# Performance work log

Measured on AMD Instinct MI355X. Metric: run time of the kernel, lower is better.

Reference implementation:

```python
import jax, jax.numpy as jnp
import numpy as np

DIM = 2240; HEADS = 20; HD = 112
B = 1; F = 8; H = 16; W = 28; S = F * H * W; ENC = 300
HID = int(3.0 * DIM)  # 6720
EPS_LN = 1e-6; EPS_RMS = 1e-5


def setup_inputs():
    ks = iter(jax.random.split(jax.random.key(0), 64))
    nrm = lambda shape, s=1.0: jax.random.normal(next(ks), shape, jnp.float32) * s
    wsc = 0.02
    inp = dict(
        hidden_states=nrm((B, S, DIM)),
        encoder_hidden_states=nrm((B, ENC, DIM)),
        timestep=nrm((B, 6 * DIM), 0.1),
        freqs_cos=nrm((1, S, 1, HD)),
        freqs_sin=nrm((1, S, 1, HD)),
        scale_shift_table=nrm((6, DIM), 1.0 / np.sqrt(DIM)),
    )
    for p in ("a1", "a2"):
        inp[p + "_qw"] = nrm((DIM, DIM), wsc); inp[p + "_qb"] = jnp.zeros((DIM,), jnp.float32)
        inp[p + "_kw"] = nrm((DIM, DIM), wsc); inp[p + "_kb"] = jnp.zeros((DIM,), jnp.float32)
        inp[p + "_vw"] = nrm((DIM, DIM), wsc); inp[p + "_vb"] = jnp.zeros((DIM,), jnp.float32)
        inp[p + "_nq"] = jnp.ones((DIM,), jnp.float32)
        inp[p + "_nk"] = jnp.ones((DIM,), jnp.float32)
        inp[p + "_ow"] = nrm((DIM, DIM), wsc); inp[p + "_ob"] = jnp.zeros((DIM,), jnp.float32)
    inp["ff_inv_w"] = nrm((1, 1, DIM, 2 * HID), wsc)
    inp["ff_inv_b"] = jnp.zeros((2 * HID,), jnp.float32)
    inp["ff_depth_w"] = nrm((3, 3, 1, 2 * HID), wsc)
    inp["ff_depth_b"] = jnp.zeros((2 * HID,), jnp.float32)
    inp["ff_point_w"] = nrm((1, 1, HID, DIM), wsc)
    inp["ff_temp_w"] = nrm((3, 1, DIM, DIM), wsc)
    inp["frames"] = F; inp["height"] = H; inp["width"] = W
    return inp


def _ln(x):  # LayerNorm, no affine (elementwise_affine=False)
    m = jnp.mean(x, -1, keepdims=True)
    v = jnp.mean((x - m) ** 2, -1, keepdims=True)
    return (x - m) * jax.lax.rsqrt(v + EPS_LN)


def _rms(x, w):  # rms_norm_across_heads on full inner dim
    return x * jax.lax.rsqrt(jnp.mean(x * x, -1, keepdims=True) + EPS_RMS) * w


def _rope(x, cos, sin):  # interleaved rotary as in SanaLinearAttnProcessor3_0
    x1, x2 = x[..., 0::2], x[..., 1::2]
    c, s = cos[..., 0::2], sin[..., 1::2]
    out = jnp.stack([x1 * c - x2 * s, x1 * s + x2 * c], axis=-1)
    return out.reshape(x.shape)


def _conv(x, k, padding, groups=1):
    return jax.lax.conv_general_dilated(
        x, k, (1, 1), padding,
        dimension_numbers=("NHWC", "HWIO", "NHWC"),
        feature_group_count=groups)


def _linear_attn(x, qw, qb, kw, kb, vw, vb, nq, nk, ow, ob, cos, sin):
    b, s, _ = x.shape
    q = jax.nn.relu(_rms(x @ qw + qb, nq)).reshape(b, s, HEADS, HD)
    k = jax.nn.relu(_rms(x @ kw + kb, nk)).reshape(b, s, HEADS, HD)
    v = (x @ vw + vb).reshape(b, s, HEADS, HD)
    qr, kr = _rope(q, cos, sin), _rope(k, cos, sin)
    ksum = jnp.sum(k, axis=1)                             # [b,h,d] (un-rotated)
    denom = jnp.einsum("bhd,bshd->bsh", ksum, q) + 1e-15  # z^{-1}
    scores = jnp.einsum("bshe,bshd->bhed", v, kr)         # [b,h,dv,d]
    out = jnp.einsum("bhed,bshd->bshe", scores, qr) / denom[..., None]
    return out.reshape(b, s, HEADS * HD) @ ow + ob


def _cross_attn(x, enc, qw, qb, kw, kb, vw, vb, nq, nk, ow, ob):
    b, s, _ = x.shape; t = enc.shape[1]
    q = _rms(x @ qw + qb, nq).reshape(b, s, HEADS, HD)
    k = _rms(enc @ kw + kb, nk).reshape(b, t, HEADS, HD)
    v = (enc @ vw + vb).reshape(b, t, HEADS, HD)
    logits = jnp.einsum("bshd,bthd->bhst", q, k) / np.sqrt(HD).astype(np.float32)
    attn = jax.nn.softmax(logits, axis=-1)
    out = jnp.einsum("bhst,bthd->bshd", attn, v).reshape(b, s, HEADS * HD)
    return out @ ow + ob


def _ff(x, inv_w, inv_b, depth_w, depth_b, point_w, temp_w, f, h, w):
    b = x.shape[0]
    y = x.reshape(b * f, h, w, DIM)
    y = jax.nn.silu(_conv(y, inv_w, "SAME") + inv_b)
    y = _conv(y, depth_w, "SAME", groups=2 * HID) + depth_b
    a, g = y[..., :HID], y[..., HID:]
    y = _conv(a * jax.nn.silu(g), point_w, "SAME")        # [bf,h,w,DIM]
    yt = y.reshape(b, f, h * w, DIM)                      # conv over frames axis
    yt = yt + _conv(yt, temp_w, ((1, 1), (0, 0)))
    return yt.reshape(b, f, h, w, DIM)


def reference(hidden_states, encoder_hidden_states, timestep, freqs_cos, freqs_sin,
              scale_shift_table,
              a1_qw, a1_qb, a1_kw, a1_kb, a1_vw, a1_vb, a1_nq, a1_nk, a1_ow, a1_ob,
              a2_qw, a2_qb, a2_kw, a2_kb, a2_vw, a2_vb, a2_nq, a2_nk, a2_ow, a2_ob,
              ff_inv_w, ff_inv_b, ff_depth_w, ff_depth_b, ff_point_w, ff_temp_w,
              frames, height, width):
    b = hidden_states.shape[0]
    mods = scale_shift_table[None] + timestep.reshape(b, 6, DIM)
    sh_msa, sc_msa, g_msa, sh_mlp, sc_mlp, g_mlp = jnp.split(mods, 6, axis=1)
    nh = _ln(hidden_states) * (1 + sc_msa) + sh_msa
    attn = _linear_attn(nh, a1_qw, a1_qb, a1_kw, a1_kb, a1_vw, a1_vb,
                        a1_nq, a1_nk, a1_ow, a1_ob, freqs_cos, freqs_sin)
    x = hidden_states + g_msa * attn
    x = x + _cross_attn(x, encoder_hidden_states, a2_qw, a2_qb, a2_kw, a2_kb,
                        a2_vw, a2_vb, a2_nq, a2_nk, a2_ow, a2_ob)
    nh = _ln(x) * (1 + sc_mlp) + sh_mlp
    ff = _ff(nh.reshape(b, frames, height, width, DIM),
             ff_inv_w, ff_inv_b, ff_depth_w, ff_depth_b, ff_point_w, ff_temp_w,
             frames, height, width)
    x = x + g_mlp * ff.reshape(b, frames * height * width, DIM)
    return x
```

## Files before the change

kernel.cpp:

```cpp
#include <hip/hip_runtime.h>

#define DIMC 2240
#define STOK 3584
#define ENCT 300
#define NH   20
#define HDIM 112
#define HID1 6720
#define HID2 13440
#define DD   (2240*2240)
#define SD   (3584*2240)

typedef short bf16x8 __attribute__((ext_vector_type(8)));
typedef float f32x4  __attribute__((ext_vector_type(4)));

__device__ __forceinline__ unsigned short f2bf(float f){
  unsigned int u = __float_as_uint(f);
  u += 0x7fffu + ((u >> 16) & 1u);
  return (unsigned short)(u >> 16);
}
__device__ __forceinline__ float bf2f(unsigned short h){
  return __uint_as_float(((unsigned int)h) << 16);
}
__device__ __forceinline__ void gl_lds16(const unsigned short* g, unsigned short* l){
  __builtin_amdgcn_global_load_lds(
      (const __attribute__((address_space(1))) unsigned int*)(const void*)g,
      (__attribute__((address_space(3))) unsigned int*)(void*)l, 16, 0, 0);
}

__global__ void cvt_k(const float4* __restrict__ src, ushort4* __restrict__ dst, int n4){
  int i = blockIdx.x*256 + threadIdx.x;
  if (i < n4){
    float4 v = src[i];
    ushort4 o; o.x = f2bf(v.x); o.y = f2bf(v.y); o.z = f2bf(v.z); o.w = f2bf(v.w);
    dst[i] = o;
  }
}

__global__ __launch_bounds__(256) void cvtT3_k(const float* __restrict__ s0,
    const float* __restrict__ s1, const float* __restrict__ s2,
    unsigned short* __restrict__ dst, int rows, int ldsrc, int c0, int nc,
    int ldd, long long dzoff){
  const float* src = (blockIdx.z == 0) ? s0 : ((blockIdx.z == 1) ? s1 : s2);
  unsigned short* d = dst + (size_t)blockIdx.z * (size_t)dzoff;
  __shared__ float tile[32][33];
  const int tx = threadIdx.x & 31, ty = threadIdx.x >> 5;
  const int colBase = blockIdx.x*32;
  #pragma unroll
  for (int i = 0; i < 4; ++i){
    int rr = blockIdx.y*32 + ty + i*8;
    int cc = colBase + tx;
    tile[ty + i*8][tx] = (cc < nc) ? src[(size_t)rr*ldsrc + c0 + cc] : 0.f;
  }
  __syncthreads();
  #pragma unroll
  for (int i = 0; i < 4; ++i){
    int n = colBase + ty + i*8;
    int k = blockIdx.y*32 + tx;
    d[(size_t)n*ldd + k] = f2bf(tile[tx][ty + i*8]);
  }
}

__global__ void zpad_k(unsigned short* __restrict__ m0, unsigned short* __restrict__ m1){
  int i = blockIdx.x*256 + threadIdx.x;
  if (i < 125440){
    reinterpret_cast<uint4*>(m0)[i] = make_uint4(0u,0u,0u,0u);
    reinterpret_cast<uint4*>(m1)[i] = make_uint4(0u,0u,0u,0u);
  }
}

__global__ void pack3_k(float* __restrict__ dst, const float* __restrict__ b0,
    const float* __restrict__ b1, const float* __restrict__ b2, int nslots){
  int i = blockIdx.x*256 + threadIdx.x;
  if (i >= nslots*2304) return;
  int slot = i / 2304, d = i - slot*2304;
  const float* src = (slot == 0) ? b0 : ((slot == 1) ? b1 : b2);
  dst[i] = (d < 2240) ? src[d] : 0.f;
}

__global__ void mods_k(const float* __restrict__ sst, const float* __restrict__ ts, float* __restrict__ mods){
  int i = blockIdx.x*256 + threadIdx.x;
  if (i < 6*DIMC) mods[i] = sst[i] + ts[i];
}

__global__ __launch_bounds__(256) void ln_mod_k(const float* __restrict__ x,
    const float* __restrict__ mods, int shj, int scj, unsigned short* __restrict__ out)
{
  const int s = blockIdx.x;
  const float4* row4 = reinterpret_cast<const float4*>(x + (size_t)s*DIMC);
  const float4* sh4 = reinterpret_cast<const float4*>(mods + shj*DIMC);
  const float4* sc4 = reinterpret_cast<const float4*>(mods + scj*DIMC);
  float sum = 0.f, sq = 0.f;
  for (int o = threadIdx.x; o < 560; o += 256){
    float4 v = row4[o];
    sum += v.x + v.y + v.z + v.w;
    sq  += v.x*v.x + v.y*v.y + v.z*v.z + v.w*v.w;
  }
  #pragma unroll
  for (int o = 32; o; o >>= 1){ sum += __shfl_down(sum, o); sq += __shfl_down(sq, o); }
  __shared__ float sA[4], sB[4];
  int w = threadIdx.x >> 6, l = threadIdx.x & 63;
  if (!l){ sA[w] = sum; sB[w] = sq; }
  __syncthreads();
  sum = sA[0]+sA[1]+sA[2]+sA[3];
  sq  = sB[0]+sB[1]+sB[2]+sB[3];
  float mean = sum * (1.f/DIMC);
  float rs = rsqrtf(sq*(1.f/DIMC) - mean*mean + 1e-6f);
  unsigned short* orow = out + (size_t)s*DIMC;
  for (int o = threadIdx.x; o < 560; o += 256){
    float4 v = row4[o], sc = sc4[o], sh = sh4[o];
    ushort4 r;
    r.x = f2bf((v.x-mean)*rs*(1.f + sc.x) + sh.x);
    r.y = f2bf((v.y-mean)*rs*(1.f + sc.y) + sh.y);
    r.z = f2bf((v.z-mean)*rs*(1.f + sc.z) + sh.z);
    r.w = f2bf((v.w-mean)*rs*(1.f + sc.w) + sh.w);
    *reinterpret_cast<ushort4*>(orow + o*4) = r;
  }
}

template<int RELU, int ROPE>
__global__ __launch_bounds__(256) void rms_bf_k(unsigned short* __restrict__ x, const float* __restrict__ nw,
    const float* __restrict__ cosb, const float* __restrict__ sinb, unsigned short* __restrict__ xr)
{
  const int s = blockIdx.x;
  unsigned short* row = x + (size_t)s*DIMC;
  float sq = 0.f;
  for (int o = threadIdx.x; o < 280; o += 256){
    uint4 v = *reinterpret_cast<const uint4*>(row + o*8);
    unsigned int uu[4] = {v.x, v.y, v.z, v.w};
    #pragma unroll
    for (int j = 0; j < 4; ++j){
      float lo = bf2f((unsigned short)(uu[j] & 0xffffu));
      float hi = bf2f((unsigned short)(uu[j] >> 16));
      sq += lo*lo + hi*hi;
    }
  }
  #pragma unroll
  for (int o = 32; o; o >>= 1) sq += __shfl_down(sq, o);
  __shared__ float sB[4];
  int w = threadIdx.x >> 6, l = threadIdx.x & 63;
  if (!l) sB[w] = sq;
  __syncthreads();
  sq = sB[0]+sB[1]+sB[2]+sB[3];
  float rs = rsqrtf(sq*(1.f/DIMC) + 1e-5f);
  for (int o = threadIdx.x; o < 280; o += 256){
    uint4 v = *reinterpret_cast<const uint4*>(row + o*8);
    unsigned int uu[4] = {v.x, v.y, v.z, v.w};
    float4 n0 = *reinterpret_cast<const float4*>(nw + o*8);
    float4 n1 = *reinterpret_cast<const float4*>(nw + o*8 + 4);
    float nn[8] = {n0.x,n0.y,n0.z,n0.w,n1.x,n1.y,n1.z,n1.w};
    float vals[8];
    #pragma unroll
    for (int j = 0; j < 4; ++j){
      vals[2*j]   = bf2f((unsigned short)(uu[j] & 0xffffu))*rs*nn[2*j];
      vals[2*j+1] = bf2f((unsigned short)(uu[j] >> 16))*rs*nn[2*j+1];
    }
    if constexpr (RELU){
      #pragma unroll
      for (int j = 0; j < 8; ++j) vals[j] = fmaxf(vals[j], 0.f);
    }
    uint4 o1;
    unsigned int* po = &o1.x;
    #pragma unroll
    for (int j = 0; j < 4; ++j)
      po[j] = (unsigned int)f2bf(vals[2*j]) | ((unsigned int)f2bf(vals[2*j+1]) << 16);
    *reinterpret_cast<uint4*>(row + o*8) = o1;
    if constexpr (ROPE){
      int jb = (o*8) % HDIM;
      uint4 o2;
      unsigned int* pr = &o2.x;
      #pragma unroll
      for (int p = 0; p < 4; ++p){
        float c  = cosb[(size_t)s*HDIM + jb + 2*p];
        float sn = sinb[(size_t)s*HDIM + jb + 2*p + 1];
        float r0 = vals[2*p]*c - vals[2*p+1]*sn;
        float r1 = vals[2*p]*sn + vals[2*p+1]*c;
        pr[p] = (unsigned int)f2bf(r0) | ((unsigned int)f2bf(r1) << 16);
      }
      *reinterpret_cast<uint4*>(xr + (size_t)s*DIMC + o*8) = o2;
    }
  }
}

template<int EPI>
__global__ __launch_bounds__(256) void gemm_bt(
  const unsigned short* __restrict__ A, const unsigned short* __restrict__ Bt,
  const float* __restrict__ bias, float* __restrict__ Cf, unsigned short* __restrict__ Cb,
  const float* __restrict__ res, const float* __restrict__ gate,
  int M, int N, int K, int ldc, int PW, int lda, int tcsh)
{
  __shared__ __align__(16) unsigned short Al[128*64];
  __shared__ __align__(16) unsigned short Bl[128*64];
  const int gx = gridDim.x, gy = gridDim.y;
  const int nwg = gx*gy;
  const int orig = blockIdx.y*gx + blockIdx.x;
  const int qq = nwg >> 3, rr = nwg & 7;
  const int xcd = orig & 7, li = orig >> 3;
  const int wg = (xcd < rr ? xcd*(qq+1) : rr*(qq+1) + (xcd-rr)*qq) + li;
  const int ppw = gy*PW;
  const int panel = wg / ppw, rm = wg - panel*ppw;
  const int mrow = rm / PW;
  const int m0 = mrow*128;
  const int n0 = (panel*PW + (rm - mrow*PW))*128;

  const int t = threadIdx.x, lane = t & 63, w = t >> 6;
  const int wr = w >> 1, wc = w & 1;
  const int l16 = lane & 15, lk = lane >> 4;

  const int lr8 = lane >> 3;
  const int sc  = (lane & 7) ^ lr8;
  const unsigned short* Aps[4];
  const unsigned short* Bps[4];
  #pragma unroll
  for (int i = 0; i < 4; ++i){
    int ar = m0 + w*32 + i*8 + lr8;
    int br = n0 + w*32 + i*8 + lr8;
    Aps[i] = A  + (size_t)min(ar, M-1)*lda + sc*8;
    Bps[i] = Bt + (size_t)br*K + sc*8;
  }
  unsigned short* Ad = Al + w*2048;
  unsigned short* Bd = Bl + w*2048;

  f32x4 acc[4][4] = {};
  for (int k0 = 0; k0 < K; k0 += 64){
    size_t aoff;
    if (tcsh){
      int sec = (k0 >= 4480) ? 2 : ((k0 >= 2240) ? 1 : 0);
      aoff = (size_t)(sec*448)*lda + (unsigned)(k0 - sec*2240);
    } else {
      aoff = (size_t)k0;
    }
    __syncthreads();
    #pragma unroll
    for (int i = 0; i < 4; ++i){
      gl_lds16(Aps[i] + aoff, Ad + i*512);
      gl_lds16(Bps[i] + k0,   Bd + i*512);
    }
    __syncthreads();
    #pragma unroll
    for (int kk = 0; kk < 2; ++kk){
      bf16x8 af[4], bfr[4];
      const int chb = (kk*4 + lk) ^ (l16 & 7);
      #pragma unroll
      for (int m = 0; m < 4; ++m)
        af[m] = *reinterpret_cast<const bf16x8*>(Al + (wr*64 + m*16 + l16)*64 + chb*8);
      #pragma unroll
      for (int n = 0; n < 4; ++n)
        bfr[n] = *reinterpret_cast<const bf16x8*>(Bl + (wc*64 + n*16 + l16)*64 + chb*8);
      #pragma unroll
      for (int m = 0; m < 4; ++m)
        #pragma unroll
        for (int n = 0; n < 4; ++n)
          acc[m][n] = __builtin_amdgcn_mfma_f32_16x16x32_bf16(af[m], bfr[n], acc[m][n], 0, 0, 0);
    }
  }

  const int rb = m0 + wr*64 + lk*4;
  const int cb = n0 + wc*64 + l16;
  #pragma unroll
  for (int m = 0; m < 4; ++m){
    #pragma unroll
    for (int r = 0; r < 4; ++r){
      int row = rb + m*16 + r;
      if (row >= M) continue;
      #pragma unroll
      for (int n = 0; n < 4; ++n){
        int col = cb + n*16;
        if (col >= N) continue;
        float v = acc[m][n][r];
        float bv = bias ? bias[col] : 0.f;
        if constexpr (EPI == 6){
          int slot = col / 2304;
          int d = col - slot*2304;
          if (d < 2240)
            Cb[(size_t)slot*ldc + (size_t)row*2240 + d] = f2bf(v + bv);
        } else {
          size_t idx = (size_t)row*ldc + col;
          if constexpr (EPI == 0){ Cf[idx] = v + bv; }
          else if constexpr (EPI == 1){ float u = v + bv; Cb[idx] = f2bf(u / (1.f + __expf(-u))); }
          else if constexpr (EPI == 2){ Cb[idx] = f2bf(v + bv); }
          else if constexpr (EPI == 3){ float u = res[idx] + gate[col]*(v + bv); Cf[idx] = u; Cb[idx] = f2bf(u); }
          else if constexpr (EPI == 4){ Cf[idx] = res[idx] + v + bv; }
          else { Cf[idx] += v; }
        }
      }
    }
  }
}

__global__ void colsum_k(const unsigned short* __restrict__ k, float* __restrict__ kpart){
  int d = blockIdx.x*256 + threadIdx.x;
  if (d >= DIMC) return;
  int ch = blockIdx.y, s0 = ch*128;
  float acc = 0.f;
  for (int s = s0; s < s0+128; ++s) acc += bf2f(k[(size_t)s*DIMC + d]);
  kpart[(size_t)ch*DIMC + d] = acc;
}
__global__ void ksumred_k(const float* __restrict__ kpart, float* __restrict__ ksum){
  int d = blockIdx.x*256 + threadIdx.x;
  if (d >= DIMC) return;
  float a = 0.f;
  for (int c = 0; c < 28; ++c) a += kpart[(size_t)c*DIMC + d];
  ksum[d] = a;
}
__global__ __launch_bounds__(256) void denom_k(const unsigned short* __restrict__ q,
    const float* __restrict__ ksum, float* __restrict__ denom)
{
  int s = blockIdx.x; int w = threadIdx.x >> 6, l = threadIdx.x & 63;
  for (int h = w; h < NH; h += 4){
    const unsigned short* qb = q + (size_t)s*DIMC + h*HDIM;
    const float* kb = ksum + h*HDIM;
    float v = bf2f(qb[l])*kb[l];
    if (l < 48) v += bf2f(qb[64+l])*kb[64+l];
    #pragma unroll
    for (int o = 32; o; o >>= 1) v += __shfl_down(v, o);
    if (!l) denom[s*NH + h] = v + 1e-15f;
  }
}

#define SLSC 136
__device__ __forceinline__ int sc_idx(int e, int s){
  return e*SLSC + (s ^ (((e >> 3) & 7) << 3));
}
__global__ __launch_bounds__(256) void scores_k(const unsigned short* __restrict__ v,
    const unsigned short* __restrict__ kr, float* __restrict__ part)
{
  const int h = blockIdx.x, ch = blockIdx.y;
  __shared__ __align__(16) unsigned short Vt[112*SLSC];
  __shared__ __align__(16) unsigned short Kt[112*SLSC];
  const int t = threadIdx.x, lane = t & 63, w = t >> 6;
  const int l16 = lane & 15, lk = lane >> 4;
  const int sbase = ch*128;

  for (int p = t; p < 1792; p += 256){
    int s = p / 14, oc = (p % 14) * 8;
    bf16x8 vv = *reinterpret_cast<const bf16x8*>(v  + (size_t)(sbase+s)*DIMC + h*HDIM + oc);
    bf16x8 kk = *reinterpret_cast<const bf16x8*>(kr + (size_t)(sbase+s)*DIMC + h*HDIM + oc);
    #pragma unroll
    for (int j = 0; j < 8; ++j){
      Vt[sc_idx(oc+j, s)] = (unsigned short)vv[j];
      Kt[sc_idx(oc+j, s)] = (unsigned short)kk[j];
    }
  }
  __syncthreads();

  f32x4 acc[2][7] = {};
  #pragma unroll
  for (int ks = 0; ks < 4; ++ks){
    const int sf = ks*32 + lk*8;
    bf16x8 bfrg[7];
    #pragma unroll
    for (int nt = 0; nt < 7; ++nt){
      int d = nt*16 + l16;
      bfrg[nt] = *reinterpret_cast<const bf16x8*>(&Kt[d*SLSC + (sf ^ (((d >> 3) & 7) << 3))]);
    }
    #pragma unroll
    for (int mi = 0; mi < 2; ++mi){
      int mt = w + mi*4;
      if (mt < 7){
        int e = mt*16 + l16;
        bf16x8 afrg = *reinterpret_cast<const bf16x8*>(&Vt[e*SLSC + (sf ^ (((e >> 3) & 7) << 3))]);
        #pragma unroll
        for (int nt = 0; nt < 7; ++nt)
          acc[mi][nt] = __builtin_amdgcn_mfma_f32_16x16x32_bf16(afrg, bfrg[nt], acc[mi][nt], 0, 0, 0);
      }
    }
  }

  float* pout = part + ((size_t)ch*NH + h)*12544;
  #pragma unroll
  for (int mi = 0; mi < 2; ++mi){
    int mt = w + mi*4;
    if (mt >= 7) continue;
    #pragma unroll
    for (int nt = 0; nt < 7; ++nt)
      #pragma unroll
      for (int r = 0; r < 4; ++r)
        pout[(size_t)(mt*16 + lk*4 + r)*HDIM + nt*16 + l16] = acc[mi][nt][r];
  }
}
__global__ void scred_k(const float* __restrict__ part, unsigned short* __restrict__ sc){
  int i = blockIdx.x*256 + threadIdx.x;
  if (i >= NH*HDIM*HDIM) return;
  float a = 0.f;
  #pragma unroll
  for (int c = 0; c < 28; ++c) a += part[(size_t)c*(NH*HDIM*HDIM) + i];
  sc[i] = f2bf(a);
}

__global__ __launch_bounds__(256) void linout_k(const unsigned short* __restrict__ qr,
    const unsigned short* __restrict__ scores, const float* __restrict__ denom,
    unsigned short* __restrict__ out)
{
  const int h = blockIdx.y;
  const int t = threadIdx.x, lane = t & 63, w = t >> 6;
  const int l16 = lane & 15, lk = lane >> 4;
  const int s0 = blockIdx.x*64 + w*16;
  const unsigned short* qrow = qr + (size_t)(s0 + l16)*DIMC + h*HDIM;
  const unsigned short* sb = scores + (size_t)h*12544;
  f32x4 acc[7] = {};
  #pragma unroll
  for (int ks = 0; ks < 4; ++ks){
    int d0 = ks*32 + lk*8;
    bf16x8 a = {};
    if (d0 < HDIM) a = *reinterpret_cast<const bf16x8*>(qrow + d0);
    #pragma unroll
    for (int nt = 0; nt < 7; ++nt){
      bf16x8 b = {};
      if (d0 < HDIM) b = *reinterpret_cast<const bf16x8*>(sb + (size_t)(nt*16 + l16)*HDIM + d0);
      acc[nt] = __builtin_amdgcn_mfma_f32_16x16x32_bf16(a, b, acc[nt], 0, 0, 0);
    }
  }
  #pragma unroll
  for (int r = 0; r < 4; ++r){
    int s = s0 + lk*4 + r;
    float dn = 1.f / denom[(size_t)s*NH + h];
    #pragma unroll
    for (int nt = 0; nt < 7; ++nt)
      out[(size_t)s*DIMC + h*HDIM + nt*16 + l16] = f2bf(acc[nt][r]*dn);
  }
}

__global__ __launch_bounds__(256) void xattn_k(
    const unsigned short* __restrict__ q,
    const unsigned short* __restrict__ k2,
    const unsigned short* __restrict__ v2,
    unsigned short* __restrict__ outb)
{
  const int h = blockIdx.y;
  const int w = threadIdx.x >> 6, lane = threadIdx.x & 63;
  const int l16 = lane & 15, lk = lane >> 4;
  const float scale = 0.09449111825230679f;

  __shared__ __align__(16) unsigned short Kl[64][136];
  __shared__ __align__(16) unsigned short Vl[112][72];
  __shared__ __align__(16) unsigned short Pl[4][16][72];

  bf16x8 qf[4];
  const unsigned short* qbase = q + (size_t)(blockIdx.x*64 + w*16 + l16)*DIMC + h*HDIM;
  #pragma unroll
  for (int c = 0; c < 4; ++c){
    int d0 = c*32 + lk*8;
    bf16x8 z = {};
    qf[c] = (d0 < HDIM) ? *reinterpret_cast<const bf16x8*>(qbase + d0) : z;
  }

  f32x4 lg[5][4] = {};
  #pragma unroll
  for (int c = 0; c < 5; ++c){
    const int kbase = c*64;
    const int nk = (c == 4) ? (ENCT - 256) : 64;
    __syncthreads();
    #pragma unroll
    for (int it = 0; it < 4; ++it){
      int li = it*256 + threadIdx.x;
      int key = li >> 4, d0 = (li & 15) << 3;
      uint4 val = make_uint4(0u,0u,0u,0u);
      if (key < nk && d0 < HDIM)
        val = *reinterpret_cast<const uint4*>(k2 + (size_t)(kbase+key)*DIMC + h*HDIM + d0);
      *reinterpret_cast<uint4*>(&Kl[key][d0]) = val;
    }
    __syncthreads();
    #pragma unroll
    for (int nt = 0; nt < 4; ++nt){
      #pragma unroll
      for (int ks = 0; ks < 4; ++ks){
        bf16x8 kf = *reinterpret_cast<const bf16x8*>(&Kl[nt*16 + l16][ks*32 + lk*8]);
        lg[c][nt] = __builtin_amdgcn_mfma_f32_16x16x32_bf16(qf[ks], kf, lg[c][nt], 0, 0, 0);
      }
    }
  }

  float mx[4] = {-3e38f, -3e38f, -3e38f, -3e38f};
  #pragma unroll
  for (int c = 0; c < 5; ++c)
    #pragma unroll
    for (int nt = 0; nt < 4; ++nt){
      bool valid = (c*64 + nt*16 + l16) < ENCT;
      #pragma unroll
      for (int r = 0; r < 4; ++r){
        float v = valid ? lg[c][nt][r]*scale : -3e38f;
        lg[c][nt][r] = v;
        mx[r] = fmaxf(mx[r], v);
      }
    }
  #pragma unroll
  for (int o = 1; o < 16; o <<= 1)
    #pragma unroll
    for (int r = 0; r < 4; ++r) mx[r] = fmaxf(mx[r], __shfl_xor(mx[r], o));
  float sm[4] = {0.f, 0.f, 0.f, 0.f};
  #pragma unroll
  for (int c = 0; c < 5; ++c)
    #pragma unroll
    for (int nt = 0; nt < 4; ++nt)
      #pragma unroll
      for (int r = 0; r < 4; ++r){
        float e = __expf(lg[c][nt][r] - mx[r]);
        lg[c][nt][r] = e;
        sm[r] += e;
      }
  #pragma unroll
  for (int o = 1; o < 16; o <<= 1)
    #pragma unroll
    for (int r = 0; r < 4; ++r) sm[r] += __shfl_xor(sm[r], o);
  float inv[4];
  #pragma unroll
  for (int r = 0; r < 4; ++r) inv[r] = 1.f / sm[r];

  f32x4 oacc[7] = {};
  #pragma unroll
  for (int c = 0; c < 5; ++c){
    const int kbase = c*64;
    const int nk = (c == 4) ? (ENCT - 256) : 64;
    __syncthreads();
    #pragma unroll
    for (int it = 0; it < 4; ++it){
      int li = it*256 + threadIdx.x;
      if (li < 896){
        int key = li/14, d0 = (li%14)*8;
        if (key < nk){
          bf16x8 vv = *reinterpret_cast<const bf16x8*>(v2 + (size_t)(kbase+key)*DIMC + h*HDIM + d0);
          #pragma unroll
          for (int j = 0; j < 8; ++j) Vl[d0+j][key] = (unsigned short)vv[j];
        } else {
          #pragma unroll
          for (int j = 0; j < 8; ++j) Vl[d0+j][key] = 0;
        }
      }
    }
    #pragma unroll
    for (int nt = 0; nt < 4; ++nt)
      #pragma unroll
      for (int r = 0; r < 4; ++r)
        Pl[w][lk*4 + r][nt*16 + l16] = f2bf(lg[c][nt][r]);
    __syncthreads();
    #pragma unroll
    for (int ks = 0; ks < 2; ++ks){
      bf16x8 pf = *reinterpret_cast<const bf16x8*>(&Pl[w][l16][ks*32 + lk*8]);
      #pragma unroll
      for (int n = 0; n < 7; ++n){
        bf16x8 vf = *reinterpret_cast<const bf16x8*>(&Vl[n*16 + l16][ks*32 + lk*8]);
        oacc[n] = __builtin_amdgcn_mfma_f32_16x16x32_bf16(pf, vf, oacc[n], 0, 0, 0);
      }
    }
  }

  const int orow = blockIdx.x*64 + w*16 + lk*4;
  #pragma unroll
  for (int n = 0; n < 7; ++n)
    #pragma unroll
    for (int r = 0; r < 4; ++r)
      outb[(size_t)(orow + r)*DIMC + h*HDIM + n*16 + l16] = f2bf(oacc[n][r]*inv[r]);
}

__global__ __launch_bounds__(256) void dw_k(const unsigned short* __restrict__ y1,
    const float* __restrict__ dw, const float* __restrict__ db, unsigned short* __restrict__ y2)
{
  int c = (blockIdx.y*256 + threadIdx.x)*2;
  if (c >= HID1) return;
  int bx = blockIdx.x;
  int xp = bx % 14;
  int yt = (bx / 14) & 3;
  int f  = bx / 56;
  int x0 = xp*2, y0 = yt*4;

  float wa[9][2], wg[9][2];
  #pragma unroll
  for (int tp = 0; tp < 9; ++tp){
    float2 va = *reinterpret_cast<const float2*>(dw + tp*HID2 + c);
    float2 vg = *reinterpret_cast<const float2*>(dw + tp*HID2 + c + HID1);
    wa[tp][0] = va.x; wa[tp][1] = va.y;
    wg[tp][0] = vg.x; wg[tp][1] = vg.y;
  }
  float2 ba = *reinterpret_cast<const float2*>(db + c);
  float2 bg = *reinterpret_cast<const float2*>(db + c + HID1);
  float a[4][2][2], g[4][2][2];
  #pragma unroll
  for (int r = 0; r < 4; ++r)
    #pragma unroll
    for (int cc = 0; cc < 2; ++cc){
      a[r][cc][0] = ba.x; a[r][cc][1] = ba.y;
      g[r][cc][0] = bg.x; g[r][cc][1] = bg.y;
    }

  #pragma unroll
  for (int dy6 = 0; dy6 < 6; ++dy6){
    int y = y0 - 1 + dy6;
    if ((unsigned)y >= 16u) continue;
    #pragma unroll
    for (int dxc = 0; dxc < 4; ++dxc){
      int x = x0 - 1 + dxc;
      if ((unsigned)x >= 28u) continue;
      size_t base = ((size_t)(f*16 + y)*28 + x)*HID2;
      unsigned int a01 = *reinterpret_cast<const unsigned int*>(y1 + base + c);
      unsigned int g01 = *reinterpret_cast<const unsigned int*>(y1 + base + c + HID1);
      float fa0 = bf2f((unsigned short)(a01 & 0xffffu));
      float fa1 = bf2f((unsigned short)(a01 >> 16));
      float fg0 = bf2f((unsigned short)(g01 & 0xffffu));
      float fg1 = bf2f((unsigned short)(g01 >> 16));
      #pragma unroll
      for (int r = 0; r < 4; ++r){
        int kdy = dy6 - r;
        if (kdy < 0 || kdy > 2) continue;
        #pragma unroll
        for (int cc = 0; cc < 2; ++cc){
          int kdx = dxc - cc;
          if (kdx < 0 || kdx > 2) continue;
          int tp = kdy*3 + kdx;
          a[r][cc][0] += fa0*wa[tp][0]; a[r][cc][1] += fa1*wa[tp][1];
          g[r][cc][0] += fg0*wg[tp][0]; g[r][cc][1] += fg1*wg[tp][1];
        }
      }
    }
  }
  #pragma unroll
  for (int r = 0; r < 4; ++r)
    #pragma unroll
    for (int cc = 0; cc < 2; ++cc){
      float s0 = g[r][cc][0] / (1.f + __expf(-g[r][cc][0]));
      float s1 = g[r][cc][1] / (1.f + __expf(-g[r][cc][1]));
      int pos = (f*16 + y0 + r)*28 + x0 + cc;
      unsigned int o = (unsigned int)f2bf(a[r][cc][0]*s0) | ((unsigned int)f2bf(a[r][cc][1]*s1) << 16);
      *reinterpret_cast<unsigned int*>(y2 + (size_t)pos*HID1 + c) = o;
    }
}

__global__ void final_k(const float* __restrict__ x2, const unsigned short* __restrict__ y3,
    const float* __restrict__ tc, const float* __restrict__ mods, float* __restrict__ out)
{
  int i4 = (blockIdx.x*256 + threadIdx.x)*4;
  if (i4 >= SD) return;
  int d = i4 % DIMC;
  float4 xv = *reinterpret_cast<const float4*>(x2 + i4);
  float4 tv = *reinterpret_cast<const float4*>(tc + i4);
  float4 gv = *reinterpret_cast<const float4*>(mods + 5*DIMC + d);
  ushort4 yv = *reinterpret_cast<const ushort4*>(y3 + i4);
  float4 o;
  o.x = xv.x + gv.x*(bf2f(yv.x) + tv.x);
  o.y = xv.y + gv.y*(bf2f(yv.y) + tv.y);
  o.z = xv.z + gv.z*(bf2f(yv.z) + tv.z);
  o.w = xv.w + gv.w*(bf2f(yv.w) + tv.w);
  *reinterpret_cast<float4*>(out + i4) = o;
}

extern "C" void kernel_launch(void* const* d_in, const int* in_sizes, int n_in,
                              void* d_out, int out_size, void* d_ws, size_t ws_size,
                              hipStream_t stream)
{
  const float* hid   = (const float*)d_in[0];
  const float* enc   = (const float*)d_in[1];
  const float* tstep = (const float*)d_in[2];
  const float* fcos  = (const float*)d_in[3];
  const float* fsin  = (const float*)d_in[4];
  const float* sst   = (const float*)d_in[5];
  const float *a1_qw=(const float*)d_in[6],  *a1_qb=(const float*)d_in[7];
  const float *a1_kw=(const float*)d_in[8],  *a1_kb=(const float*)d_in[9];
  const float *a1_vw=(const float*)d_in[10], *a1_vb=(const float*)d_in[11];
  const float *a1_nq=(const float*)d_in[12], *a1_nk=(const float*)d_in[13];
  const float *a1_ow=(const float*)d_in[14], *a1_ob=(const float*)d_in[15];
  const float *a2_qw=(const float*)d_in[16], *a2_qb=(const float*)d_in[17];
  const float *a2_kw=(const float*)d_in[18], *a2_kb=(const float*)d_in[19];
  const float *a2_vw=(const float*)d_in[20], *a2_vb=(const float*)d_in[21];
  const float *a2_nq=(const float*)d_in[22], *a2_nk=(const float*)d_in[23];
  const float *a2_ow=(const float*)d_in[24], *a2_ob=(const float*)d_in[25];
  const float *ff_inv_w=(const float*)d_in[26], *ff_inv_b=(const float*)d_in[27];
  const float *ff_dw=(const float*)d_in[28], *ff_db=(const float*)d_in[29];
  const float *ff_pw=(const float*)d_in[30];
  const float *ff_tw=(const float*)d_in[31];
  float* out = (float*)d_out;

  const size_t SLOTB = (size_t)SD*2;
  char* ws = (char*)d_ws;
  size_t off = 0;
  auto alloc = [&](size_t n){ void* p = ws + off; off += (n + 255) & ~(size_t)255; return p; };

  char* P = (char*)alloc(6*SLOTB);
  float* x1    = (float*)alloc((size_t)SD*4);
  unsigned short* nh2b = (unsigned short*)alloc(SLOTB);
  float* x2    = (float*)alloc((size_t)SD*4);
  unsigned short* k2b = (unsigned short*)alloc((size_t)ENCT*DIMC*2);
  unsigned short* v2b = (unsigned short*)alloc((size_t)ENCT*DIMC*2);
  unsigned short* encb = (unsigned short*)alloc((size_t)ENCT*DIMC*2);
  float* modsb = (float*)alloc(6*DIMC*4);
  float* ksum  = (float*)alloc(DIMC*4);
  float* kpart = (float*)alloc((size_t)28*DIMC*4);
  float* denom = (float*)alloc((size_t)STOK*NH*4);
  unsigned short* scorb = (unsigned short*)alloc((size_t)NH*HDIM*HDIM*2);
  float* bias3 = (float*)alloc(3*2304*4);
  unsigned short* Wbig = (unsigned short*)alloc((size_t)6912*DIMC*2);

  unsigned short* P0 = (unsigned short*)P;
  unsigned short* P1 = (unsigned short*)(P + 1*SLOTB);
  unsigned short* P2 = (unsigned short*)(P + 2*SLOTB);
  unsigned short* P3 = (unsigned short*)(P + 3*SLOTB);
  unsigned short* P4 = (unsigned short*)(P + 4*SLOTB);
  unsigned short* P5 = (unsigned short*)(P + 5*SLOTB);
  unsigned short* nhb = P0;
  unsigned short* y1b = P0;
  unsigned short* y2b = (unsigned short*)x1;
  unsigned short* y3pad = P0;
  unsigned short* y3  = y3pad + (size_t)448*DIMC;
  float* tc = (float*)(P + 2*SLOTB);
  float* spart = (float*)P1;

  auto cvt = [&](const float* s, unsigned short* d, size_t n){
    int n4 = (int)(n/4);
    cvt_k<<<dim3((n4+255)/256), 256, 0, stream>>>((const float4*)s, (ushort4*)d, n4);
  };
  auto cvtT3 = [&](const float* s0, const float* s1, const float* s2, unsigned short* d,
                   int rows, int ldsrc, int c0, int nc, int ncPad, int ldd, long long dzoff, int nz){
    cvtT3_k<<<dim3(ncPad/32, rows/32, nz), 256, 0, stream>>>(s0, s1, s2, d, rows, ldsrc, c0, nc, ldd, dzoff);
  };
  auto gemm_grid = [&](int M, int Npad){ return dim3(Npad/128, (M+127)/128); };

  mods_k<<<dim3((6*DIMC+255)/256), 256, 0, stream>>>(sst, tstep, modsb);
  cvt(enc, encb, (size_t)ENCT*DIMC);

  ln_mod_k<<<dim3(STOK), 256, 0, stream>>>(hid, modsb, 0, 1, nhb);
  pack3_k<<<dim3((3*2304+255)/256), 256, 0, stream>>>(bias3, a1_qb, a1_kb, a1_vb, 3);
  cvtT3(a1_qw, a1_kw, a1_vw, Wbig, DIMC, DIMC, 0, DIMC, 2304, DIMC, (long long)2304*DIMC, 3);
  gemm_bt<6><<<gemm_grid(STOK, 6912), 256, 0, stream>>>(nhb, Wbig, bias3, nullptr, P1,
                                                        nullptr, nullptr, STOK, 6912, DIMC, SD, 6, DIMC, 0);
  rms_bf_k<1,1><<<dim3(STOK), 256, 0, stream>>>(P1, a1_nq, fcos, fsin, P4);
  rms_bf_k<1,1><<<dim3(STOK), 256, 0, stream>>>(P2, a1_nk, fcos, fsin, P5);
  colsum_k<<<dim3(9, 28), 256, 0, stream>>>(P2, kpart);
  ksumred_k<<<dim3(9), 256, 0, stream>>>(kpart, ksum);
  denom_k<<<dim3(STOK), 256, 0, stream>>>(P1, ksum, denom);
  scores_k<<<dim3(NH, 28), 256, 0, stream>>>(P3, P5, spart);
  scred_k<<<dim3((NH*HDIM*HDIM+255)/256), 256, 0, stream>>>(spart, scorb);
  linout_k<<<dim3(STOK/64, NH), 256, 0, stream>>>(P4, scorb, denom, P1);
  dim3 gMN = gemm_grid(STOK, 2304);
  cvtT3(a1_ow, a1_ow, a1_ow, Wbig, DIMC, DIMC, 0, DIMC, 2304, DIMC, 0, 1);
  gemm_bt<3><<<gMN, 256, 0, stream>>>(P1, Wbig, a1_ob, x1, P2, hid, modsb + 2*DIMC, STOK, DIMC, DIMC, DIMC, 6, DIMC, 0);

  cvtT3(a2_qw, a2_qw, a2_qw, Wbig, DIMC, DIMC, 0, DIMC, 2304, DIMC, 0, 1);
  gemm_bt<2><<<gMN, 256, 0, stream>>>(P2, Wbig, a2_qb, nullptr, P3, nullptr, nullptr, STOK, DIMC, DIMC, DIMC, 6, DIMC, 0);
  pack3_k<<<dim3((2*2304+255)/256), 256, 0, stream>>>(bias3, a2_kb, a2_vb, a2_vb, 2);
  cvtT3(a2_kw, a2_vw, a2_vw, Wbig, DIMC, DIMC, 0, DIMC, 2304, DIMC, (long long)2304*DIMC, 2);
  gemm_bt<6><<<gemm_grid(ENCT, 4608), 256, 0, stream>>>(encb, Wbig, bias3, nullptr, k2b,
                                                        nullptr, nullptr, ENCT, 4608, DIMC, ENCT*DIMC, 6, DIMC, 0);
  rms_bf_k<0,0><<<dim3(STOK), 256, 0, stream>>>(P3, a2_nq, nullptr, nullptr, nullptr);
  rms_bf_k<0,0><<<dim3(ENCT), 256, 0, stream>>>(k2b, a2_nk, nullptr, nullptr, nullptr);
  xattn_k<<<dim3(STOK/64, NH), 256, 0, stream>>>(P3, k2b, v2b, P4);
  cvtT3(a2_ow, a2_ow, a2_ow, Wbig, DIMC, DIMC, 0, DIMC, 2304, DIMC, 0, 1);
  gemm_bt<4><<<gMN, 256, 0, stream>>>(P4, Wbig, a2_ob, x2, nullptr, x1, nullptr, STOK, DIMC, DIMC, DIMC, 6, DIMC, 0);

  ln_mod_k<<<dim3(STOK), 256, 0, stream>>>(x2, modsb, 3, 4, nh2b);
  for (int q = 0; q < 2; ++q){
    int c0 = q*6720;
    cvtT3(ff_inv_w, ff_inv_w, ff_inv_w, Wbig, DIMC, HID2, c0, 6720, 6912, DIMC, 0, 1);
    gemm_bt<1><<<gemm_grid(STOK, 6912), 256, 0, stream>>>(nh2b, Wbig, ff_inv_b + c0, nullptr, y1b + c0,
                                                          nullptr, nullptr, STOK, 6720, DIMC, HID2, 6, DIMC, 0);
  }
  dw_k<<<dim3(448, 14), 256, 0, stream>>>(y1b, ff_dw, ff_db, y2b);
  zpad_k<<<dim3(490), 256, 0, stream>>>(y3pad, y3pad + (size_t)(448 + STOK)*DIMC);
  cvtT3(ff_pw, ff_pw, ff_pw, Wbig, HID1, DIMC, 0, DIMC, 2304, HID1, 0, 1);
  gemm_bt<2><<<gMN, 256, 0, stream>>>(y2b, Wbig, nullptr, nullptr, y3,
                                      nullptr, nullptr, STOK, DIMC, HID1, DIMC, 2, HID1, 0);
  cvtT3(ff_tw, ff_tw + (size_t)DD, ff_tw + (size_t)2*DD, Wbig,
        DIMC, DIMC, 0, DIMC, 2304, 6720, 2240LL, 3);
  gemm_bt<0><<<gMN, 256, 0, stream>>>(y3pad, Wbig, nullptr, tc, nullptr, nullptr, nullptr,
                                      STOK, DIMC, 6720, DIMC, 6, DIMC, 1);

  final_k<<<dim3((SD/4+255)/256), 256, 0, stream>>>(x2, y3, tc, modsb, out);
}
```

Measured before the change: 1.360 ms.

## Fuse final residual into temporal GEMM, batch weight conversions, widen depthwise tile

The final elementwise kernel is folded into the temporal-conv GEMM through a new epilogue that reads the bf16 pointwise output and writes the gated residual straight to the output. This removes the fp32 temp buffer and one full pass over the activations. Three separate weight transpose-convert launches (a1_ow, a2_qw, a2_ow) are merged into one launch that fills three Wbig slots. The depthwise conv tile is widened from 2 to 4 columns per thread to reuse loaded neighbours, at the cost of more registers.

```diff
diff --git a/kernel.cpp b/kernel.cpp
--- a/kernel.cpp
+++ b/kernel.cpp
@@ -280,6 +280,7 @@
           else if constexpr (EPI == 2){ Cb[idx] = f2bf(v + bv); }
           else if constexpr (EPI == 3){ float u = res[idx] + gate[col]*(v + bv); Cf[idx] = u; Cb[idx] = f2bf(u); }
           else if constexpr (EPI == 4){ Cf[idx] = res[idx] + v + bv; }
+          else if constexpr (EPI == 7){ Cf[idx] = res[idx] + gate[col]*(bf2f(Cb[idx]) + v); }
           else { Cf[idx] += v; }
         }
       }
@@ -558,10 +559,10 @@
   int c = (blockIdx.y*256 + threadIdx.x)*2;
   if (c >= HID1) return;
   int bx = blockIdx.x;
-  int xp = bx % 14;
-  int yt = (bx / 14) & 3;
-  int f  = bx / 56;
-  int x0 = xp*2, y0 = yt*4;
+  int xq = bx % 7;
+  int yt = (bx / 7) & 3;
+  int f  = bx / 28;
+  int x0 = xq*4, y0 = yt*4;
 
   float wa[9][2], wg[9][2];
   #pragma unroll
@@ -573,11 +574,11 @@
   }
   float2 ba = *reinterpret_cast<const float2*>(db + c);
   float2 bg = *reinterpret_cast<const float2*>(db + c + HID1);
-  float a[4][2][2], g[4][2][2];
+  float a[4][4][2], g[4][4][2];
   #pragma unroll
   for (int r = 0; r < 4; ++r)
     #pragma unroll
-    for (int cc = 0; cc < 2; ++cc){
+    for (int cc = 0; cc < 4; ++cc){
       a[r][cc][0] = ba.x; a[r][cc][1] = ba.y;
       g[r][cc][0] = bg.x; g[r][cc][1] = bg.y;
     }
@@ -587,7 +588,7 @@
     int y = y0 - 1 + dy6;
     if ((unsigned)y >= 16u) continue;
     #pragma unroll
-    for (int dxc = 0; dxc < 4; ++dxc){
+    for (int dxc = 0; dxc < 6; ++dxc){
       int x = x0 - 1 + dxc;
       if ((unsigned)x >= 28u) continue;
       size_t base = ((size_t)(f*16 + y)*28 + x)*HID2;
@@ -602,7 +603,7 @@
         int kdy = dy6 - r;
         if (kdy < 0 || kdy > 2) continue;
         #pragma unroll
-        for (int cc = 0; cc < 2; ++cc){
+        for (int cc = 0; cc < 4; ++cc){
           int kdx = dxc - cc;
           if (kdx < 0 || kdx > 2) continue;
           int tp = kdy*3 + kdx;
@@ -615,31 +616,13 @@
   #pragma unroll
   for (int r = 0; r < 4; ++r)
     #pragma unroll
-    for (int cc = 0; cc < 2; ++cc){
+    for (int cc = 0; cc < 4; ++cc){
       float s0 = g[r][cc][0] / (1.f + __expf(-g[r][cc][0]));
       float s1 = g[r][cc][1] / (1.f + __expf(-g[r][cc][1]));
       int pos = (f*16 + y0 + r)*28 + x0 + cc;
       unsigned int o = (unsigned int)f2bf(a[r][cc][0]*s0) | ((unsigned int)f2bf(a[r][cc][1]*s1) << 16);
       *reinterpret_cast<unsigned int*>(y2 + (size_t)pos*HID1 + c) = o;
     }
-}
-
-__global__ void final_k(const float* __restrict__ x2, const unsigned short* __restrict__ y3,
-    const float* __restrict__ tc, const float* __restrict__ mods, float* __restrict__ out)
-{
-  int i4 = (blockIdx.x*256 + threadIdx.x)*4;
-  if (i4 >= SD) return;
-  int d = i4 % DIMC;
-  float4 xv = *reinterpret_cast<const float4*>(x2 + i4);
-  float4 tv = *reinterpret_cast<const float4*>(tc + i4);
-  float4 gv = *reinterpret_cast<const float4*>(mods + 5*DIMC + d);
-  ushort4 yv = *reinterpret_cast<const ushort4*>(y3 + i4);
-  float4 o;
-  o.x = xv.x + gv.x*(bf2f(yv.x) + tv.x);
-  o.y = xv.y + gv.y*(bf2f(yv.y) + tv.y);
-  o.z = xv.z + gv.z*(bf2f(yv.z) + tv.z);
-  o.w = xv.w + gv.w*(bf2f(yv.w) + tv.w);
-  *reinterpret_cast<float4*>(out + i4) = o;
 }
 
 extern "C" void kernel_launch(void* const* d_in, const int* in_sizes, int n_in,
@@ -699,7 +682,6 @@
   unsigned short* y2b = (unsigned short*)x1;
   unsigned short* y3pad = P0;
   unsigned short* y3  = y3pad + (size_t)448*DIMC;
-  float* tc = (float*)(P + 2*SLOTB);
   float* spart = (float*)P1;
 
   auto cvt = [&](const float* s, unsigned short* d, size_t n){
@@ -711,13 +693,14 @@
     cvtT3_k<<<dim3(ncPad/32, rows/32, nz), 256, 0, stream>>>(s0, s1, s2, d, rows, ldsrc, c0, nc, ldd, dzoff);
   };
   auto gemm_grid = [&](int M, int Npad){ return dim3(Npad/128, (M+127)/128); };
+  const long long WSLOT = (long long)2304*DIMC;
 
   mods_k<<<dim3((6*DIMC+255)/256), 256, 0, stream>>>(sst, tstep, modsb);
   cvt(enc, encb, (size_t)ENCT*DIMC);
 
   ln_mod_k<<<dim3(STOK), 256, 0, stream>>>(hid, modsb, 0, 1, nhb);
   pack3_k<<<dim3((3*2304+255)/256), 256, 0, stream>>>(bias3, a1_qb, a1_kb, a1_vb, 3);
-  cvtT3(a1_qw, a1_kw, a1_vw, Wbig, DIMC, DIMC, 0, DIMC, 2304, DIMC, (long long)2304*DIMC, 3);
+  cvtT3(a1_qw, a1_kw, a1_vw, Wbig, DIMC, DIMC, 0, DIMC, 2304, DIMC, WSLOT, 3);
   gemm_bt<6><<<gemm_grid(STOK, 6912), 256, 0, stream>>>(nhb, Wbig, bias3, nullptr, P1,
                                                         nullptr, nullptr, STOK, 6912, DIMC, SD, 6, DIMC, 0);
   rms_bf_k<1,1><<<dim3(STOK), 256, 0, stream>>>(P1, a1_nq, fcos, fsin, P4);
@@ -729,20 +712,18 @@
   scred_k<<<dim3((NH*HDIM*HDIM+255)/256), 256, 0, stream>>>(spart, scorb);
   linout_k<<<dim3(STOK/64, NH), 256, 0, stream>>>(P4, scorb, denom, P1);
   dim3 gMN = gemm_grid(STOK, 2304);
-  cvtT3(a1_ow, a1_ow, a1_ow, Wbig, DIMC, DIMC, 0, DIMC, 2304, DIMC, 0, 1);
+  cvtT3(a1_ow, a2_qw, a2_ow, Wbig, DIMC, DIMC, 0, DIMC, 2304, DIMC, WSLOT, 3);
   gemm_bt<3><<<gMN, 256, 0, stream>>>(P1, Wbig, a1_ob, x1, P2, hid, modsb + 2*DIMC, STOK, DIMC, DIMC, DIMC, 6, DIMC, 0);
 
-  cvtT3(a2_qw, a2_qw, a2_qw, Wbig, DIMC, DIMC, 0, DIMC, 2304, DIMC, 0, 1);
-  gemm_bt<2><<<gMN, 256, 0, stream>>>(P2, Wbig, a2_qb, nullptr, P3, nullptr, nullptr, STOK, DIMC, DIMC, DIMC, 6, DIMC, 0);
+  gemm_bt<2><<<gMN, 256, 0, stream>>>(P2, Wbig + WSLOT, a2_qb, nullptr, P3, nullptr, nullptr, STOK, DIMC, DIMC, DIMC, 6, DIMC, 0);
   pack3_k<<<dim3((2*2304+255)/256), 256, 0, stream>>>(bias3, a2_kb, a2_vb, a2_vb, 2);
-  cvtT3(a2_kw, a2_vw, a2_vw, Wbig, DIMC, DIMC, 0, DIMC, 2304, DIMC, (long long)2304*DIMC, 2);
+  cvtT3(a2_kw, a2_vw, a2_vw, Wbig, DIMC, DIMC, 0, DIMC, 2304, DIMC, WSLOT, 2);
   gemm_bt<6><<<gemm_grid(ENCT, 4608), 256, 0, stream>>>(encb, Wbig, bias3, nullptr, k2b,
                                                         nullptr, nullptr, ENCT, 4608, DIMC, ENCT*DIMC, 6, DIMC, 0);
   rms_bf_k<0,0><<<dim3(STOK), 256, 0, stream>>>(P3, a2_nq, nullptr, nullptr, nullptr);
   rms_bf_k<0,0><<<dim3(ENCT), 256, 0, stream>>>(k2b, a2_nk, nullptr, nullptr, nullptr);
   xattn_k<<<dim3(STOK/64, NH), 256, 0, stream>>>(P3, k2b, v2b, P4);
-  cvtT3(a2_ow, a2_ow, a2_ow, Wbig, DIMC, DIMC, 0, DIMC, 2304, DIMC, 0, 1);
-  gemm_bt<4><<<gMN, 256, 0, stream>>>(P4, Wbig, a2_ob, x2, nullptr, x1, nullptr, STOK, DIMC, DIMC, DIMC, 6, DIMC, 0);
+  gemm_bt<4><<<gMN, 256, 0, stream>>>(P4, Wbig + 2*WSLOT, a2_ob, x2, nullptr, x1, nullptr, STOK, DIMC, DIMC, DIMC, 6, DIMC, 0);
 
   ln_mod_k<<<dim3(STOK), 256, 0, stream>>>(x2, modsb, 3, 4, nh2b);
   for (int q = 0; q < 2; ++q){
@@ -751,15 +732,13 @@
     gemm_bt<1><<<gemm_grid(STOK, 6912), 256, 0, stream>>>(nh2b, Wbig, ff_inv_b + c0, nullptr, y1b + c0,
                                                           nullptr, nullptr, STOK, 6720, DIMC, HID2, 6, DIMC, 0);
   }
-  dw_k<<<dim3(448, 14), 256, 0, stream>>>(y1b, ff_dw, ff_db, y2b);
+  dw_k<<<dim3(224, 14), 256, 0, stream>>>(y1b, ff_dw, ff_db, y2b);
   zpad_k<<<dim3(490), 256, 0, stream>>>(y3pad, y3pad + (size_t)(448 + STOK)*DIMC);
   cvtT3(ff_pw, ff_pw, ff_pw, Wbig, HID1, DIMC, 0, DIMC, 2304, HID1, 0, 1);
   gemm_bt<2><<<gMN, 256, 0, stream>>>(y2b, Wbig, nullptr, nullptr, y3,
                                       nullptr, nullptr, STOK, DIMC, HID1, DIMC, 2, HID1, 0);
   cvtT3(ff_tw, ff_tw + (size_t)DD, ff_tw + (size_t)2*DD, Wbig,
         DIMC, DIMC, 0, DIMC, 2304, 6720, 2240LL, 3);
-  gemm_bt<0><<<gMN, 256, 0, stream>>>(y3pad, Wbig, nullptr, tc, nullptr, nullptr, nullptr,
-                                      STOK, DIMC, 6720, DIMC, 6, DIMC, 1);
-
-  final_k<<<dim3((SD/4+255)/256), 256, 0, stream>>>(x2, y3, tc, modsb, out);
-}
+  gemm_bt<7><<<gMN, 256, 0, stream>>>(y3pad, Wbig, nullptr, out, y3, x2, modsb + 5*DIMC,
+                                      STOK, DIMC, 6720, DIMC, 2, DIMC, 1);
+}
```

Measured after the change: 1.358 ms. No clear change (-0.1%).
